# Kernel tuning notes

Hardware: AMD Instinct MI355X
Metric: run time of the kernel (lower is better)

Reference implementation:

```python
import jax, jax.numpy as jnp
import numpy as np

B, N, T, F_, H, PATCH, OUT_LEN, TOPK = 4, 325, 288, 64, 8, 12, 288, 5
FPH = F_ // H  # features per head
L = T // PATCH  # patched sequence length (even, so irfft round-trips)


def setup_inputs() -> dict:
    key = jax.random.key(0)
    ks = jax.random.split(key, 15)
    s = 0.05  # small weight scale to keep softmaxes well-conditioned
    return {
        "Q_in": jax.random.normal(ks[0], (B, N, T, F_), jnp.float32),
        "K_in": jax.random.normal(ks[1], (B, N, T, F_), jnp.float32),
        "V_in": jax.random.normal(ks[2], (B, N, T, F_), jnp.float32),
        "adj": jax.random.uniform(ks[3], (N, N), jnp.float32),
        "Wq": jax.random.normal(ks[4], (H, F_, 1, PATCH), jnp.float32) * s,
        "Wk": jax.random.normal(ks[5], (H, F_, 1, PATCH), jnp.float32) * s,
        "Wv": jax.random.normal(ks[6], (FPH, F_, 1, 1), jnp.float32) * s,
        "Wout_map": jax.random.normal(ks[7], (F_, FPH), jnp.float32) * s,
        "gQ1": jax.random.normal(ks[8], (1, OUT_LEN), jnp.float32) * s,
        "gQ2": jax.random.normal(ks[9], (128, F_), jnp.float32) * s,
        "gK1": jax.random.normal(ks[10], (1, OUT_LEN), jnp.float32) * s,
        "gK2": jax.random.normal(ks[11], (128, F_), jnp.float32) * s,
        "gWa": jax.random.normal(ks[12], (128, 128), jnp.float32) * s,
        "gWg": jax.random.normal(ks[13], (F_, 128), jnp.float32) * s,
        "gWout": jax.random.normal(ks[14], (128, F_), jnp.float32) * s,
    }


def _forward(Q_in, K_in, V_in, adj, Wq, Wk, Wv, Wout_map,
             gQ1, gQ2, gK1, gK2, gWa, gWg, gWout):
    # ---- cal_QKV: patchified conv projections -> FFT autocorrelation ----
    # Conv2d(F->H, kernel (1,PATCH), stride (1,PATCH)) == per-patch einsum
    xq = Q_in.reshape(B, N, L, PATCH, F_)
    xk = K_in.reshape(B, N, L, PATCH, F_)
    q = jnp.einsum('bnlpf,hfp->bnhl', xq, Wq[:, :, 0, :])  # (B,N,H,L)
    k = jnp.einsum('bnlpf,hfp->bnhl', xk, Wk[:, :, 0, :])  # (B,N,H,L)
    qf = jnp.fft.rfft(q, axis=-1)
    kf = jnp.fft.rfft(k, axis=-1)
    corr = jnp.fft.irfft(qf * jnp.conj(kf), n=L, axis=-1)  # (B,N,H,L)

    # values: Conv2d(F->FPH, 1x1) then repeat to F channels
    v_small = jnp.einsum('bntf,gf->bntg', V_in, Wv[:, :, 0, 0])  # (B,N,T,FPH)
    v_rep = jnp.tile(v_small, (1, 1, 1, H)).reshape(B, N, T, FPH, H)
    v = jnp.transpose(v_rep, (0, 1, 3, 4, 2))  # (B,N,FPH,H,T)

    # ---- time_delay_agg_full2: per-head topk delays, gather, weighted sum ----
    weights, delay = jax.lax.top_k(corr, TOPK)  # (B,N,H,TOPK)
    delay = delay * PATCH
    tmp_corr = jax.nn.softmax(weights, axis=-1)  # (B,N,H,TOPK)
    tt = jnp.arange(OUT_LEN)
    agg = jnp.zeros((B, N, FPH, H, OUT_LEN), v.dtype)
    for i in range(TOPK):  # small fixed loop over top-k delays
        # gather from doubled time axis == modular indexing into length-T axis
        idx = (delay[:, :, None, :, i, None] + tt) % T  # (B,N,1,H,OUT_LEN)
        idx = jnp.broadcast_to(idx, (B, N, FPH, H, OUT_LEN))
        pattern = jnp.take_along_axis(v, idx, axis=-1)
        agg = agg + pattern * tmp_corr[:, :, None, :, i, None]
    out = agg.mean(axis=3)  # mean over heads -> (B,N,FPH,OUT_LEN)
    # out_mapping Linear(FPH->F) on time-major layout; permutes cancel -> (B,N,OUT_LEN,F)
    out = jnp.einsum('bnct,fc->bntf', out, Wout_map)

    # ---- GCN aggregation with inline full attention ----
    xp = jnp.transpose(out, (0, 1, 3, 2))  # (B,N,F,OUT_LEN)
    qg = jax.nn.relu(jnp.einsum('bnfl,l->bnf', xp, gQ1[0]))
    Qg = jnp.einsum('bnf,hf->bnh', qg, gQ2)  # (B,N,128)
    kg = jax.nn.relu(jnp.einsum('bnfl,l->bnf', xp, gK1[0]))
    Kg = jnp.einsum('bnf,hf->bnh', kg, gK2)  # (B,N,128)
    A = jnp.einsum('bnh,hg,bmg->bnm', Qg, gWa, Kg)  # (B,N,N)
    A = jax.nn.softmax(A, axis=-1)
    adj2 = A * adj[None]  # (B,N,N)
    xw = jnp.einsum('bntf,fh->bnth', out, gWg)  # (B,N,OUT_LEN,128)
    xw = jax.nn.gelu(jnp.einsum('bnm,bmth->bnth', adj2, xw), approximate=False)
    new_values = jnp.einsum('bnth,hf->bntf', xw, gWout)  # (B,N,OUT_LEN,F)
    return new_values, delay, tmp_corr, adj2


def reference(Q_in, K_in, V_in, adj, Wq, Wk, Wv, Wout_map,
              gQ1, gQ2, gK1, gK2, gWa, gWg, gWout):
    return _forward(Q_in, K_in, V_in, adj, Wq, Wk, Wv, Wout_map,
                    gQ1, gQ2, gK1, gK2, gWa, gWg, gWout)
```

## Files before the change

### kernel.cpp

```cpp
#include <hip/hip_runtime.h>
#include <math.h>

#define B_ 4
#define N_ 325
#define T_ 288
#define F2_ 64
#define H_ 8
#define PATCH_ 12
#define L_ 24
#define TOPK_ 5
#define BN_ (B_*N_)

#define NV_LEN 23961600
#define OQ   0
#define OKk  249600
#define OVS  499200
#define OS   3494400
#define OQG  3868800
#define OKG2 4035200
#define ODELAY 23961600
#define OTC    24013600
#define OADJ2  24065600

#define WU    0
#define WSQ   374400
#define WSK   375700
#define WWSUM 377000
#define WGW   377064

__device__ __forceinline__ float reduce8(float acc[8], int lane) {
#pragma unroll
  for (int h = 0; h < 8; ++h) {
    acc[h] += __shfl_xor(acc[h], 32);
    acc[h] += __shfl_xor(acc[h], 16);
    acc[h] += __shfl_xor(acc[h], 8);
  }
  int g = lane >> 3;
  float s0 = (g & 1) ? acc[1] : acc[0];
  float s1 = (g & 1) ? acc[3] : acc[2];
  float s2 = (g & 1) ? acc[5] : acc[4];
  float s3 = (g & 1) ? acc[7] : acc[6];
  float t0 = (g & 2) ? s1 : s0;
  float t1 = (g & 2) ? s3 : s2;
  float v  = (g & 4) ? t1 : t0;
  v += __shfl_xor(v, 4);
  v += __shfl_xor(v, 2);
  v += __shfl_xor(v, 1);
  return v;
}

__global__ __launch_bounds__(128) void k0_wsum_gw(const float* __restrict__ Wout_map,
                                                  const float* __restrict__ gWg,
                                                  float* __restrict__ ws) {
  __shared__ float wsum_s[64];
  int tid = threadIdx.x;
  if (tid < 64) {
    float a = 0.f;
#pragma unroll
    for (int c = 0; c < 8; ++c) a += Wout_map[tid * 8 + c];
    wsum_s[tid] = a;
    ws[WWSUM + tid] = a;
  }
  __syncthreads();
  float g = 0.f;
  for (int f = 0; f < 64; ++f) g += wsum_s[f] * gWg[f * 128 + tid];
  ws[WGW + tid] = g;
}

__global__ __launch_bounds__(256) void k1_qkproj(const float* __restrict__ Qin,
                                                 const float* __restrict__ Kin,
                                                 const float* __restrict__ Wq,
                                                 const float* __restrict__ Wk,
                                                 float* outbuf) {
  __shared__ float wt[6144];
  int bn = blockIdx.x;
  int tid = threadIdx.x;
  int lane = tid & 63;
  int w = tid >> 6;
  for (int phase = 0; phase < 2; ++phase) {
    const float* W = phase ? Wk : Wq;
    const float* X = phase ? Kin : Qin;
    float* qout = outbuf + (phase ? OKk : OQ);
    if (phase) __syncthreads();
    for (int i = tid; i < 6144; i += 256) {
      int h = i / 768, r = i % 768, f = r / 12, p = r % 12;
      wt[h * 768 + p * 64 + f] = W[i];
    }
    __syncthreads();
    for (int l = w; l < 24; l += 4) {
      float acc[8] = {0, 0, 0, 0, 0, 0, 0, 0};
      const float* xrow = X + ((size_t)bn * 288 + l * 12) * 64;
#pragma unroll
      for (int p = 0; p < 12; ++p) {
        float x = xrow[p * 64 + lane];
#pragma unroll
        for (int h = 0; h < 8; ++h) acc[h] += x * wt[h * 768 + p * 64 + lane];
      }
      float v = reduce8(acc, lane);
      if ((lane & 7) == 0) {
        int h = lane >> 3;
        qout[(bn * 8 + h) * 24 + l] = v;
      }
    }
  }
}

__global__ __launch_bounds__(256) void k2_vproj(const float* __restrict__ Vin,
                                                const float* __restrict__ Wv,
                                                float* outbuf) {
  __shared__ float wv[512];
  int bn = blockIdx.x, tid = threadIdx.x, lane = tid & 63, w = tid >> 6;
  wv[tid] = Wv[tid];
  wv[tid + 256] = Wv[tid + 256];
  __syncthreads();
  float* vs = outbuf + OVS;
  for (int t = w; t < 288; t += 4) {
    float x = Vin[((size_t)bn * 288 + t) * 64 + lane];
    float acc[8];
#pragma unroll
    for (int h = 0; h < 8; ++h) acc[h] = x * wv[h * 64 + lane];
    float v = reduce8(acc, lane);
    if ((lane & 7) == 0) vs[(bn * 8 + (lane >> 3)) * 288 + t] = v;
  }
}

__global__ __launch_bounds__(256) void k3_corr_topk(const float* buf, float* out) {
  int row = blockIdx.x * 256 + threadIdx.x;
  if (row >= BN_ * H_) return;
  const float* q = buf + OQ + row * 24;
  const float* k = buf + OKk + row * 24;
  float qv[24], kv[24];
#pragma unroll
  for (int m = 0; m < 24; ++m) { qv[m] = q[m]; kv[m] = k[m]; }
  float corr[24];
#pragma unroll
  for (int l = 0; l < 24; ++l) {
    float a = 0.f;
#pragma unroll
    for (int m = 0; m < 24; ++m) a += qv[m] * kv[(m - l + 24) % 24];
    corr[l] = a;
  }
  int idx[5]; float wv_[5];
  int i0 = -1, i1 = -1, i2 = -1, i3 = -1;
#pragma unroll
  for (int j = 0; j < 5; ++j) {
    float best = -3.0e38f; int bi = 0;
#pragma unroll
    for (int l = 0; l < 24; ++l) {
      bool taken = (l == i0) | (l == i1) | (l == i2) | (l == i3);
      if (!taken && corr[l] > best) { best = corr[l]; bi = l; }
    }
    idx[j] = bi; wv_[j] = best;
    if (j == 0) i0 = bi; else if (j == 1) i1 = bi;
    else if (j == 2) i2 = bi; else if (j == 3) i3 = bi;
  }
  float mx = wv_[0];
  float e[5], ssum = 0.f;
#pragma unroll
  for (int j = 0; j < 5; ++j) { e[j] = expf(wv_[j] - mx); ssum += e[j]; }
  float inv = 1.0f / ssum;
#pragma unroll
  for (int j = 0; j < 5; ++j) {
    out[ODELAY + row * 5 + j] = (float)(idx[j] * 12);
    out[OTC + row * 5 + j] = e[j] * inv;
  }
}

__global__ __launch_bounds__(320) void k4_s(const float* __restrict__ gQ1,
                                            const float* __restrict__ gK1,
                                            float* out, float* __restrict__ ws) {
  int bn = blockIdx.x, tid = threadIdx.x;
  __shared__ float tc_s[40];
  __shared__ int d_s[40];
  __shared__ float r1[5], r2[5];
  if (tid < 40) {
    tc_s[tid] = out[OTC + bn * 40 + tid];
    d_s[tid] = (int)(out[ODELAY + bn * 40 + tid] + 0.5f);
  }
  __syncthreads();
  int t = tid;
  float sval = 0.f;
  if (t < 288) {
    const float* vsb = out + OVS + (size_t)bn * 8 * 288;
    float acc = 0.f;
#pragma unroll
    for (int h = 0; h < 8; ++h) {
      const float* vr = vsb + h * 288;
#pragma unroll
      for (int i = 0; i < 5; ++i) {
        int ix = d_s[h * 5 + i] + t;
        if (ix >= 288) ix -= 288;
        acc += tc_s[h * 5 + i] * vr[ix];
      }
    }
    sval = 0.125f * acc;
    out[OS + bn * 288 + t] = sval;
  }
  float a1 = (t < 288) ? sval * gQ1[t] : 0.f;
  float a2 = (t < 288) ? sval * gK1[t] : 0.f;
#pragma unroll
  for (int off = 32; off; off >>= 1) { a1 += __shfl_xor(a1, off); a2 += __shfl_xor(a2, off); }
  int w = tid >> 6, lane = tid & 63;
  if (lane == 0) { r1[w] = a1; r2[w] = a2; }
  __syncthreads();
  if (tid == 0) {
    float s1 = 0.f, s2 = 0.f;
#pragma unroll
    for (int i = 0; i < 5; ++i) { s1 += r1[i]; s2 += r2[i]; }
    ws[WSQ + bn] = s1;
    ws[WSK + bn] = s2;
  }
}

__global__ __launch_bounds__(128) void k5_qkg(const float* __restrict__ gQ2,
                                              const float* __restrict__ gK2,
                                              const float* __restrict__ gWa,
                                              float* out, const float* __restrict__ ws) {
  int bn = blockIdx.x, h = threadIdx.x;
  __shared__ float qg[64], kg[64], kgv[128];
  float sq = ws[WSQ + bn], sk = ws[WSK + bn];
  if (h < 64) {
    float wsm = ws[WWSUM + h];
    qg[h] = fmaxf(wsm * sq, 0.f);
    kg[h] = fmaxf(wsm * sk, 0.f);
  }
  __syncthreads();
  float Qv = 0.f, Kv = 0.f;
  const float4* gq4 = (const float4*)(gQ2 + h * 64);
  const float4* gk4 = (const float4*)(gK2 + h * 64);
  const float4* qg4 = (const float4*)qg;
  const float4* kg4 = (const float4*)kg;
#pragma unroll
  for (int i = 0; i < 16; ++i) {
    float4 a = gq4[i], x = qg4[i];
    Qv += a.x * x.x + a.y * x.y + a.z * x.z + a.w * x.w;
    float4 b = gk4[i], y = kg4[i];
    Kv += b.x * y.x + b.y * y.y + b.z * y.z + b.w * y.w;
  }
  kgv[h] = Kv;
  __syncthreads();
  float K2v = 0.f;
  const float4* wa4 = (const float4*)(gWa + h * 128);
  const float4* kv4 = (const float4*)kgv;
#pragma unroll
  for (int i = 0; i < 32; ++i) {
    float4 a = wa4[i], x = kv4[i];
    K2v += a.x * x.x + a.y * x.y + a.z * x.z + a.w * x.w;
  }
  out[OQG + bn * 128 + h] = Qv;
  out[OKG2 + bn * 128 + h] = K2v;
}

__global__ __launch_bounds__(384) void k6_attn(const float* __restrict__ adj, float* out) {
  int bn = blockIdx.x, b = bn / N_, n = bn % N_, tid = threadIdx.x;
  __shared__ float qs[128];
  __shared__ float red1[6], red2[6];
  if (tid < 128) qs[tid] = out[OQG + bn * 128 + tid];
  __syncthreads();
  int m = tid;
  float logit = -3.0e38f;
  if (m < N_) {
    const float4* kr = (const float4*)(out + OKG2 + ((size_t)b * N_ + m) * 128);
    const float4* q4 = (const float4*)qs;
    float a = 0.f;
#pragma unroll
    for (int i = 0; i < 32; ++i) {
      float4 x = kr[i], y = q4[i];
      a += x.x * y.x + x.y * y.y + x.z * y.z + x.w * y.w;
    }
    logit = a;
  }
  float v = logit;
#pragma unroll
  for (int off = 32; off; off >>= 1) v = fmaxf(v, __shfl_xor(v, off));
  int w = tid >> 6, lane = tid & 63;
  if (lane == 0) red1[w] = v;
  __syncthreads();
  float mx = red1[0];
#pragma unroll
  for (int i = 1; i < 6; ++i) mx = fmaxf(mx, red1[i]);
  float ev = (m < N_) ? expf(logit - mx) : 0.f;
  float sv = ev;
#pragma unroll
  for (int off = 32; off; off >>= 1) sv += __shfl_xor(sv, off);
  if (lane == 0) red2[w] = sv;
  __syncthreads();
  float total = 0.f;
#pragma unroll
  for (int i = 0; i < 6; ++i) total += red2[i];
  if (m < N_) out[OADJ2 + (size_t)bn * N_ + m] = (ev / total) * adj[n * N_ + m];
}

__global__ __launch_bounds__(320) void k7_u(const float* out, float* __restrict__ ws) {
  int bn = blockIdx.x, b = bn / N_, tid = threadIdx.x;
  __shared__ float arow[N_];
  for (int i = tid; i < N_; i += 320) arow[i] = out[OADJ2 + (size_t)bn * N_ + i];
  __syncthreads();
  if (tid < 288) {
    const float* sb = out + OS + (size_t)b * N_ * 288 + tid;
    float acc = 0.f;
    for (int m = 0; m < N_; ++m) acc += arow[m] * sb[(size_t)m * 288];
    ws[WU + bn * 288 + tid] = acc;
  }
}

__global__ __launch_bounds__(256) void k8_final(const float* __restrict__ gWout,
                                                const float* __restrict__ ws,
                                                float* __restrict__ out) {
  __shared__ float wo[128 * 64];
  __shared__ float pl[32 * 130];
  __shared__ float gwl[128];
  __shared__ float ul[32];
  int blk = blockIdx.x;
  int bn = blk / 9, t0 = (blk % 9) * 32;
  int tid = threadIdx.x;
  const float4* src = (const float4*)gWout;
  float4* dst = (float4*)wo;
  for (int i = tid; i < 2048; i += 256) dst[i] = src[i];
  if (tid < 128) gwl[tid] = ws[WGW + tid];
  if (tid < 32) ul[tid] = ws[WU + bn * 288 + t0 + tid];
  __syncthreads();
#pragma unroll
  for (int j = 0; j < 16; ++j) {
    int i = tid + j * 256;
    int t = i >> 7, h = i & 127;
    float x = ul[t] * gwl[h];
    pl[t * 130 + h] = 0.5f * x * (1.0f + erff(x * 0.7071067811865475f));
  }
  __syncthreads();
  int tq = tid >> 4, fq = tid & 15;
  float4 acc0 = {0, 0, 0, 0}, acc1 = {0, 0, 0, 0};
#pragma unroll 8
  for (int h = 0; h < 128; ++h) {
    float4 wv = *(const float4*)&wo[h * 64 + fq * 4];
    float p0 = pl[tq * 130 + h];
    float p1 = pl[(tq + 16) * 130 + h];
    acc0.x += p0 * wv.x; acc0.y += p0 * wv.y; acc0.z += p0 * wv.z; acc0.w += p0 * wv.w;
    acc1.x += p1 * wv.x; acc1.y += p1 * wv.y; acc1.z += p1 * wv.z; acc1.w += p1 * wv.w;
  }
  size_t base = ((size_t)bn * 288 + t0) * 64;
  *(float4*)&out[base + (size_t)tq * 64 + fq * 4] = acc0;
  *(float4*)&out[base + (size_t)(tq + 16) * 64 + fq * 4] = acc1;
}

extern "C" void kernel_launch(void* const* d_in, const int* in_sizes, int n_in,
                              void* d_out, int out_size, void* d_ws, size_t ws_size,
                              hipStream_t stream) {
  const float* Qin = (const float*)d_in[0];
  const float* Kin = (const float*)d_in[1];
  const float* Vin = (const float*)d_in[2];
  const float* adj = (const float*)d_in[3];
  const float* Wq  = (const float*)d_in[4];
  const float* Wk  = (const float*)d_in[5];
  const float* Wv  = (const float*)d_in[6];
  const float* Wout_map = (const float*)d_in[7];
  const float* gQ1 = (const float*)d_in[8];
  const float* gQ2 = (const float*)d_in[9];
  const float* gK1 = (const float*)d_in[10];
  const float* gK2 = (const float*)d_in[11];
  const float* gWa = (const float*)d_in[12];
  const float* gWg = (const float*)d_in[13];
  const float* gWout = (const float*)d_in[14];
  float* out = (float*)d_out;
  float* ws = (float*)d_ws;

  k0_wsum_gw<<<1, 128, 0, stream>>>(Wout_map, gWg, ws);
  k1_qkproj<<<BN_, 256, 0, stream>>>(Qin, Kin, Wq, Wk, out);
  k2_vproj<<<BN_, 256, 0, stream>>>(Vin, Wv, out);
  k3_corr_topk<<<(BN_ * H_ + 255) / 256, 256, 0, stream>>>(out, out);
  k4_s<<<BN_, 320, 0, stream>>>(gQ1, gK1, out, ws);
  k5_qkg<<<BN_, 128, 0, stream>>>(gQ2, gK2, gWa, out, ws);
  k6_attn<<<BN_, 384, 0, stream>>>(adj, out);
  k7_u<<<BN_, 320, 0, stream>>>(out, ws);
  k8_final<<<BN_ * 9, 256, 0, stream>>>(gWout, ws, out);
}
```

Baseline: 750.4 us.

## Fuse QK projection with correlation/top-k and V projection with delay aggregation

Weight transposition for the Q/K patch projections moves into the prep kernel. Projection, circular correlation and top-k now run in one kernel per (b,n), with q/k held in shared memory and float4 loads. The V projection is fused with the time-delay aggregation and gQ1/gK1 reductions, keeping the per-head values in shared memory instead of a global round trip. This removes two launches and the intermediate global buffers. The fused kernels keep weights in registers, which raises register pressure, and the top-k step now runs on only 8 threads per block.

```diff
diff --git a/kernel.cpp b/kernel.cpp
--- a/kernel.cpp
+++ b/kernel.cpp
@@ -12,9 +12,8 @@
 #define BN_ (B_*N_)
 
 #define NV_LEN 23961600
-#define OQ   0
-#define OKk  249600
-#define OVS  499200
+#define OW2Q 499200
+#define OW2K 505344
 #define OS   3494400
 #define OQG  3868800
 #define OKG2 4035200
@@ -28,30 +27,12 @@
 #define WWSUM 377000
 #define WGW   377064
 
-__device__ __forceinline__ float reduce8(float acc[8], int lane) {
-#pragma unroll
-  for (int h = 0; h < 8; ++h) {
-    acc[h] += __shfl_xor(acc[h], 32);
-    acc[h] += __shfl_xor(acc[h], 16);
-    acc[h] += __shfl_xor(acc[h], 8);
-  }
-  int g = lane >> 3;
-  float s0 = (g & 1) ? acc[1] : acc[0];
-  float s1 = (g & 1) ? acc[3] : acc[2];
-  float s2 = (g & 1) ? acc[5] : acc[4];
-  float s3 = (g & 1) ? acc[7] : acc[6];
-  float t0 = (g & 2) ? s1 : s0;
-  float t1 = (g & 2) ? s3 : s2;
-  float v  = (g & 4) ? t1 : t0;
-  v += __shfl_xor(v, 4);
-  v += __shfl_xor(v, 2);
-  v += __shfl_xor(v, 1);
-  return v;
-}
-
-__global__ __launch_bounds__(128) void k0_wsum_gw(const float* __restrict__ Wout_map,
-                                                  const float* __restrict__ gWg,
-                                                  float* __restrict__ ws) {
+__global__ __launch_bounds__(128) void k0_prep(const float* __restrict__ Wout_map,
+                                               const float* __restrict__ gWg,
+                                               const float* __restrict__ Wq,
+                                               const float* __restrict__ Wk,
+                                               float* __restrict__ ws,
+                                               float* __restrict__ out) {
   __shared__ float wsum_s[64];
   int tid = threadIdx.x;
   if (tid < 64) {
@@ -65,148 +46,158 @@
   float g = 0.f;
   for (int f = 0; f < 64; ++f) g += wsum_s[f] * gWg[f * 128 + tid];
   ws[WGW + tid] = g;
-}
-
-__global__ __launch_bounds__(256) void k1_qkproj(const float* __restrict__ Qin,
-                                                 const float* __restrict__ Kin,
-                                                 const float* __restrict__ Wq,
-                                                 const float* __restrict__ Wk,
-                                                 float* outbuf) {
-  __shared__ float wt[6144];
-  int bn = blockIdx.x;
-  int tid = threadIdx.x;
-  int lane = tid & 63;
-  int w = tid >> 6;
-  for (int phase = 0; phase < 2; ++phase) {
-    const float* W = phase ? Wk : Wq;
-    const float* X = phase ? Kin : Qin;
-    float* qout = outbuf + (phase ? OKk : OQ);
-    if (phase) __syncthreads();
-    for (int i = tid; i < 6144; i += 256) {
-      int h = i / 768, r = i % 768, f = r / 12, p = r % 12;
-      wt[h * 768 + p * 64 + f] = W[i];
-    }
-    __syncthreads();
-    for (int l = w; l < 24; l += 4) {
-      float acc[8] = {0, 0, 0, 0, 0, 0, 0, 0};
-      const float* xrow = X + ((size_t)bn * 288 + l * 12) * 64;
-#pragma unroll
-      for (int p = 0; p < 12; ++p) {
-        float x = xrow[p * 64 + lane];
-#pragma unroll
-        for (int h = 0; h < 8; ++h) acc[h] += x * wt[h * 768 + p * 64 + lane];
+  for (int i = tid; i < 6144; i += 128) {
+    int h = i / 768, r = i % 768, p = r >> 6, f = r & 63;
+    int src = h * 768 + f * 12 + p;
+    out[OW2Q + i] = Wq[src];
+    out[OW2K + i] = Wk[src];
+  }
+}
+
+__global__ __launch_bounds__(256, 2) void k1_fused(const float* __restrict__ Qin,
+                                                   const float* __restrict__ Kin,
+                                                   float* out) {
+  __shared__ float qs[8][24], ks[8][24], cs[8][24];
+  int bn = blockIdx.x, tid = threadIdx.x, lane = tid & 63, w = tid >> 6;
+  int h0 = 2 * w, h1 = 2 * w + 1;
+  float4 wq0[3], wq1[3], wk0[3], wk1[3];
+#pragma unroll
+  for (int c = 0; c < 3; ++c) {
+    wq0[c] = *(const float4*)&out[OW2Q + h0 * 768 + c * 256 + lane * 4];
+    wq1[c] = *(const float4*)&out[OW2Q + h1 * 768 + c * 256 + lane * 4];
+    wk0[c] = *(const float4*)&out[OW2K + h0 * 768 + c * 256 + lane * 4];
+    wk1[c] = *(const float4*)&out[OW2K + h1 * 768 + c * 256 + lane * 4];
+  }
+  const float* Qb = Qin + (size_t)bn * 18432;
+  const float* Kb = Kin + (size_t)bn * 18432;
+#pragma unroll 2
+  for (int l = 0; l < 24; ++l) {
+    float4 xq[3], xk[3];
+#pragma unroll
+    for (int c = 0; c < 3; ++c) {
+      xq[c] = *(const float4*)&Qb[l * 768 + c * 256 + lane * 4];
+      xk[c] = *(const float4*)&Kb[l * 768 + c * 256 + lane * 4];
+    }
+    float aq0 = 0.f, aq1 = 0.f, ak0 = 0.f, ak1 = 0.f;
+#pragma unroll
+    for (int c = 0; c < 3; ++c) {
+      aq0 += xq[c].x * wq0[c].x + xq[c].y * wq0[c].y + xq[c].z * wq0[c].z + xq[c].w * wq0[c].w;
+      aq1 += xq[c].x * wq1[c].x + xq[c].y * wq1[c].y + xq[c].z * wq1[c].z + xq[c].w * wq1[c].w;
+      ak0 += xk[c].x * wk0[c].x + xk[c].y * wk0[c].y + xk[c].z * wk0[c].z + xk[c].w * wk0[c].w;
+      ak1 += xk[c].x * wk1[c].x + xk[c].y * wk1[c].y + xk[c].z * wk1[c].z + xk[c].w * wk1[c].w;
+    }
+#pragma unroll
+    for (int off = 32; off; off >>= 1) {
+      aq0 += __shfl_xor(aq0, off);
+      aq1 += __shfl_xor(aq1, off);
+      ak0 += __shfl_xor(ak0, off);
+      ak1 += __shfl_xor(ak1, off);
+    }
+    if (lane == 0) {
+      qs[h0][l] = aq0; qs[h1][l] = aq1;
+      ks[h0][l] = ak0; ks[h1][l] = ak1;
+    }
+  }
+  __syncthreads();
+  if (tid < 192) {
+    int h = tid / 24, l = tid % 24;
+    float a = 0.f;
+#pragma unroll
+    for (int m = 0; m < 24; ++m) a += qs[h][m] * ks[h][(m - l + 24) % 24];
+    cs[h][l] = a;
+  }
+  __syncthreads();
+  if (tid < 8) {
+    int h = tid;
+    float corr[24];
+#pragma unroll
+    for (int l = 0; l < 24; ++l) corr[l] = cs[h][l];
+    int idx[5]; float wv_[5];
+    int i0 = -1, i1 = -1, i2 = -1, i3 = -1;
+#pragma unroll
+    for (int j = 0; j < 5; ++j) {
+      float best = -3.0e38f; int bi = 0;
+#pragma unroll
+      for (int l = 0; l < 24; ++l) {
+        bool taken = (l == i0) | (l == i1) | (l == i2) | (l == i3);
+        if (!taken && corr[l] > best) { best = corr[l]; bi = l; }
       }
-      float v = reduce8(acc, lane);
-      if ((lane & 7) == 0) {
-        int h = lane >> 3;
-        qout[(bn * 8 + h) * 24 + l] = v;
-      }
-    }
-  }
-}
-
-__global__ __launch_bounds__(256) void k2_vproj(const float* __restrict__ Vin,
+      idx[j] = bi; wv_[j] = best;
+      if (j == 0) i0 = bi; else if (j == 1) i1 = bi;
+      else if (j == 2) i2 = bi; else if (j == 3) i3 = bi;
+    }
+    float mx = wv_[0];
+    float e[5], ssum = 0.f;
+#pragma unroll
+    for (int j = 0; j < 5; ++j) { e[j] = expf(wv_[j] - mx); ssum += e[j]; }
+    float inv = 1.0f / ssum;
+    int row = bn * 8 + h;
+#pragma unroll
+    for (int j = 0; j < 5; ++j) {
+      out[ODELAY + row * 5 + j] = (float)(idx[j] * 12);
+      out[OTC + row * 5 + j] = e[j] * inv;
+    }
+  }
+}
+
+__global__ __launch_bounds__(256, 4) void k2_vs(const float* __restrict__ Vin,
                                                 const float* __restrict__ Wv,
-                                                float* outbuf) {
-  __shared__ float wv[512];
-  int bn = blockIdx.x, tid = threadIdx.x, lane = tid & 63, w = tid >> 6;
-  wv[tid] = Wv[tid];
-  wv[tid + 256] = Wv[tid + 256];
-  __syncthreads();
-  float* vs = outbuf + OVS;
-  for (int t = w; t < 288; t += 4) {
-    float x = Vin[((size_t)bn * 288 + t) * 64 + lane];
-    float acc[8];
-#pragma unroll
-    for (int h = 0; h < 8; ++h) acc[h] = x * wv[h * 64 + lane];
-    float v = reduce8(acc, lane);
-    if ((lane & 7) == 0) vs[(bn * 8 + (lane >> 3)) * 288 + t] = v;
-  }
-}
-
-__global__ __launch_bounds__(256) void k3_corr_topk(const float* buf, float* out) {
-  int row = blockIdx.x * 256 + threadIdx.x;
-  if (row >= BN_ * H_) return;
-  const float* q = buf + OQ + row * 24;
-  const float* k = buf + OKk + row * 24;
-  float qv[24], kv[24];
-#pragma unroll
-  for (int m = 0; m < 24; ++m) { qv[m] = q[m]; kv[m] = k[m]; }
-  float corr[24];
-#pragma unroll
-  for (int l = 0; l < 24; ++l) {
-    float a = 0.f;
-#pragma unroll
-    for (int m = 0; m < 24; ++m) a += qv[m] * kv[(m - l + 24) % 24];
-    corr[l] = a;
-  }
-  int idx[5]; float wv_[5];
-  int i0 = -1, i1 = -1, i2 = -1, i3 = -1;
-#pragma unroll
-  for (int j = 0; j < 5; ++j) {
-    float best = -3.0e38f; int bi = 0;
-#pragma unroll
-    for (int l = 0; l < 24; ++l) {
-      bool taken = (l == i0) | (l == i1) | (l == i2) | (l == i3);
-      if (!taken && corr[l] > best) { best = corr[l]; bi = l; }
-    }
-    idx[j] = bi; wv_[j] = best;
-    if (j == 0) i0 = bi; else if (j == 1) i1 = bi;
-    else if (j == 2) i2 = bi; else if (j == 3) i3 = bi;
-  }
-  float mx = wv_[0];
-  float e[5], ssum = 0.f;
-#pragma unroll
-  for (int j = 0; j < 5; ++j) { e[j] = expf(wv_[j] - mx); ssum += e[j]; }
-  float inv = 1.0f / ssum;
-#pragma unroll
-  for (int j = 0; j < 5; ++j) {
-    out[ODELAY + row * 5 + j] = (float)(idx[j] * 12);
-    out[OTC + row * 5 + j] = e[j] * inv;
-  }
-}
-
-__global__ __launch_bounds__(320) void k4_s(const float* __restrict__ gQ1,
-                                            const float* __restrict__ gK1,
-                                            float* out, float* __restrict__ ws) {
-  int bn = blockIdx.x, tid = threadIdx.x;
+                                                const float* __restrict__ gQ1,
+                                                const float* __restrict__ gK1,
+                                                float* out, float* __restrict__ ws) {
+  __shared__ float vs[8][288];
   __shared__ float tc_s[40];
   __shared__ int d_s[40];
-  __shared__ float r1[5], r2[5];
+  __shared__ float r1[4], r2[4];
+  int bn = blockIdx.x, tid = threadIdx.x, lane = tid & 63, w = tid >> 6;
+  int f4 = lane & 15, tof = lane >> 4;
+  int h0 = 2 * w, h1 = 2 * w + 1;
   if (tid < 40) {
     tc_s[tid] = out[OTC + bn * 40 + tid];
     d_s[tid] = (int)(out[ODELAY + bn * 40 + tid] + 0.5f);
   }
-  __syncthreads();
-  int t = tid;
-  float sval = 0.f;
-  if (t < 288) {
-    const float* vsb = out + OVS + (size_t)bn * 8 * 288;
+  float4 wv0 = *(const float4*)&Wv[h0 * 64 + f4 * 4];
+  float4 wv1 = *(const float4*)&Wv[h1 * 64 + f4 * 4];
+  const float* Vb = Vin + (size_t)bn * 18432;
+#pragma unroll 4
+  for (int t0 = 0; t0 < 288; t0 += 4) {
+    int t = t0 + tof;
+    float4 x = *(const float4*)&Vb[t * 64 + f4 * 4];
+    float a0 = x.x * wv0.x + x.y * wv0.y + x.z * wv0.z + x.w * wv0.w;
+    float a1 = x.x * wv1.x + x.y * wv1.y + x.z * wv1.z + x.w * wv1.w;
+#pragma unroll
+    for (int off = 8; off; off >>= 1) {
+      a0 += __shfl_xor(a0, off);
+      a1 += __shfl_xor(a1, off);
+    }
+    if (f4 == 0) { vs[h0][t] = a0; vs[h1][t] = a1; }
+  }
+  __syncthreads();
+  float p1 = 0.f, p2 = 0.f;
+  for (int t = tid; t < 288; t += 256) {
     float acc = 0.f;
 #pragma unroll
     for (int h = 0; h < 8; ++h) {
-      const float* vr = vsb + h * 288;
 #pragma unroll
       for (int i = 0; i < 5; ++i) {
         int ix = d_s[h * 5 + i] + t;
         if (ix >= 288) ix -= 288;
-        acc += tc_s[h * 5 + i] * vr[ix];
+        acc += tc_s[h * 5 + i] * vs[h][ix];
       }
     }
-    sval = 0.125f * acc;
+    float sval = 0.125f * acc;
     out[OS + bn * 288 + t] = sval;
-  }
-  float a1 = (t < 288) ? sval * gQ1[t] : 0.f;
-  float a2 = (t < 288) ? sval * gK1[t] : 0.f;
-#pragma unroll
-  for (int off = 32; off; off >>= 1) { a1 += __shfl_xor(a1, off); a2 += __shfl_xor(a2, off); }
-  int w = tid >> 6, lane = tid & 63;
-  if (lane == 0) { r1[w] = a1; r2[w] = a2; }
+    p1 += sval * gQ1[t];
+    p2 += sval * gK1[t];
+  }
+#pragma unroll
+  for (int off = 32; off; off >>= 1) { p1 += __shfl_xor(p1, off); p2 += __shfl_xor(p2, off); }
+  if (lane == 0) { r1[w] = p1; r2[w] = p2; }
   __syncthreads();
   if (tid == 0) {
     float s1 = 0.f, s2 = 0.f;
 #pragma unroll
-    for (int i = 0; i < 5; ++i) { s1 += r1[i]; s2 += r2[i]; }
+    for (int i = 0; i < 4; ++i) { s1 += r1[i]; s2 += r2[i]; }
     ws[WSQ + bn] = s1;
     ws[WSK + bn] = s2;
   }
@@ -299,6 +290,7 @@
   if (tid < 288) {
     const float* sb = out + OS + (size_t)b * N_ * 288 + tid;
     float acc = 0.f;
+#pragma unroll 8
     for (int m = 0; m < N_; ++m) acc += arow[m] * sb[(size_t)m * 288];
     ws[WU + bn * 288 + tid] = acc;
   }
@@ -364,11 +356,9 @@
   float* out = (float*)d_out;
   float* ws = (float*)d_ws;
 
-  k0_wsum_gw<<<1, 128, 0, stream>>>(Wout_map, gWg, ws);
-  k1_qkproj<<<BN_, 256, 0, stream>>>(Qin, Kin, Wq, Wk, out);
-  k2_vproj<<<BN_, 256, 0, stream>>>(Vin, Wv, out);
-  k3_corr_topk<<<(BN_ * H_ + 255) / 256, 256, 0, stream>>>(out, out);
-  k4_s<<<BN_, 320, 0, stream>>>(gQ1, gK1, out, ws);
+  k0_prep<<<1, 128, 0, stream>>>(Wout_map, gWg, Wq, Wk, ws, out);
+  k1_fused<<<BN_, 256, 0, stream>>>(Qin, Kin, out);
+  k2_vs<<<BN_, 256, 0, stream>>>(Vin, Wv, gQ1, gK1, out, ws);
   k5_qkg<<<BN_, 128, 0, stream>>>(gQ2, gK2, gWa, out, ws);
   k6_attn<<<BN_, 384, 0, stream>>>(adj, out);
   k7_u<<<BN_, 320, 0, stream>>>(out, ws);
```

Result: faster. 651.6 us (-13.2%).
